# Performance work log

Hardware: AMD Instinct MI355X
Metric: run time of the kernel (lower is better)

The kernel has to match this reference:

```python
import jax, jax.numpy as jnp
import numpy as np

BLOCK_SIZE = 256


def setup_inputs() -> dict:
    key = jax.random.key(0)
    k1, k2, k3, k4 = jax.random.split(key, 4)
    B, T, C, H = 512, 256, 384, 64
    x = jax.random.normal(k1, (B, T, C), dtype=jnp.float32)
    Wk = jax.random.normal(k2, (H, C), dtype=jnp.float32) * (1.0 / np.sqrt(C))
    Wq = jax.random.normal(k3, (H, C), dtype=jnp.float32) * (1.0 / np.sqrt(C))
    Wv = jax.random.normal(k4, (H, C), dtype=jnp.float32) * (1.0 / np.sqrt(C))
    return {"x": x, "Wk": Wk, "Wq": Wq, "Wv": Wv}


def reference(x, Wk, Wq, Wv):
    # x: [B, T, C]; Wk/Wq/Wv: [H, C] (torch nn.Linear weight layout, bias=False)
    B, T, C = x.shape
    H = Wk.shape[0]
    k = jnp.einsum('btc,hc->bth', x, Wk)
    q = jnp.einsum('btc,hc->bth', x, Wq)
    v = jnp.einsum('btc,hc->bth', x, Wv)
    scale = 1.0 / jnp.sqrt(jnp.float32(H))
    scores = jnp.einsum('bqh,bkh->bqk', q, k) * scale  # [B, T, T]
    causal = jnp.tril(jnp.ones((T, T), dtype=bool))
    scores = jnp.where(causal, scores, -jnp.inf)
    weights = jax.nn.softmax(scores, axis=-1)
    # dropout is identity in eval mode
    out = jnp.einsum('bqk,bkh->bqh', weights, v)  # [B, T, H]
    return out
```

## Files before the change

kernel.cpp:

```cpp
#include <hip/hip_runtime.h>
#include <hip/hip_bf16.h>
#include <math.h>

#define TT 256
#define CC 384
#define HH 64

typedef float v4f   __attribute__((ext_vector_type(4)));
typedef short short8 __attribute__((ext_vector_type(8)));

#define MFMA(a, b, c) __builtin_amdgcn_mfma_f32_16x16x32_bf16((a), (b), (c), 0, 0, 0)

__device__ __forceinline__ unsigned short f2bf(float f) {
    unsigned int u = __float_as_uint(f);
    u += 0x7FFFu + ((u >> 16) & 1u);
    return (unsigned short)(u >> 16);
}

__device__ __forceinline__ ushort4 f2bf4(float4 f) {
    union { __hip_bfloat162 h2[2]; ushort4 u4; } cv;
    cv.h2[0] = __float22bfloat162_rn(make_float2(f.x, f.y));
    cv.h2[1] = __float22bfloat162_rn(make_float2(f.z, f.w));
    return cv.u4;
}

#define KLOOP_BARRIER() do {                                   \
    asm volatile("s_waitcnt lgkmcnt(0)" ::: "memory");         \
    __builtin_amdgcn_s_barrier();                              \
    __builtin_amdgcn_sched_barrier(0);                         \
} while (0)

#define QSCALE 0.18033688f

#define WST 0
#define KF  6144
#define VF  22528
#define SMU 38912

__global__ __launch_bounds__(512)
void prep_w(const float* __restrict__ Wkp, const float* __restrict__ Wqp,
            const float* __restrict__ Wvp, unsigned short* __restrict__ wf)
{
    const int idx  = blockIdx.x * 512 + threadIdx.x;
    const int lane = idx & 63;
    const int fn   = idx >> 6;
    const int nt   = fn % 12;
    const int s    = fn / 12;
    const int col  = lane & 15, quad = lane >> 4;
    const float* src = (nt < 4) ? Wqp : (nt < 8) ? Wkp : Wvp;
    const int h  = (nt & 3) * 16 + col;
    const int c0 = s * 32 + quad * 8;
    union { ushort4 u[2]; short8 s8; } pk;
    pk.u[0] = f2bf4(*(const float4*)(src + (size_t)h * CC + c0));
    pk.u[1] = f2bf4(*(const float4*)(src + (size_t)h * CC + c0 + 4));
    *(short8*)(wf + (size_t)idx * 8) = pk.s8;
}

__global__ __launch_bounds__(512, 4)
void fused_attn(const float* __restrict__ x, const unsigned short* __restrict__ wf,
                float* __restrict__ out)
{
    __shared__ unsigned short sm[SMU];
    const int tid  = threadIdx.x;
    const int wave = tid >> 6;
    const int lane = tid & 63;
    const int col  = lane & 15;
    const int quad = lane >> 4;
    const int b    = blockIdx.x;

    short8 aq0A, aq1A, aq0B, aq1B;

    #pragma unroll 1
    for (int half = 0; half < 2; ++half) {
        const int rb = half ? (7 - wave) : wave;
        const float* xrow = x + ((size_t)b * 256 + half * 128 + rb * 16 + col) * CC
                              + quad * 8;

        v4f acc[12];
        #pragma unroll
        for (int j = 0; j < 12; ++j) acc[j] = (v4f){0.f, 0.f, 0.f, 0.f};

        float4 xA0 = *(const float4*)(xrow);
        float4 xA1 = *(const float4*)(xrow + 4);
        short8 wA0 = *(const short8*)(wf + (size_t)tid * 8);
        short8 wA1;
        if (tid < 256) wA1 = *(const short8*)(wf + (size_t)(512 + tid) * 8);

        #pragma unroll
        for (int s = 0; s < 12; ++s) {
            float4 xB0, xB1; short8 wB0, wB1;
            if (s < 11) {
                xB0 = *(const float4*)(xrow + (s + 1) * 32);
                xB1 = *(const float4*)(xrow + (s + 1) * 32 + 4);
                wB0 = *(const short8*)(wf + ((size_t)(s + 1) * 768 + tid) * 8);
                if (tid < 256)
                    wB1 = *(const short8*)(wf + ((size_t)(s + 1) * 768 + 512 + tid) * 8);
            }
            KLOOP_BARRIER();
            *(short8*)&sm[WST + tid * 8] = wA0;
            if (tid < 256)
                *(short8*)&sm[WST + (512 + tid) * 8] = wA1;
            KLOOP_BARRIER();
            union { ushort4 u[2]; short8 s8; } pk;
            pk.u[0] = f2bf4(xA0); pk.u[1] = f2bf4(xA1);
            const short8 a = pk.s8;
            #pragma unroll
            for (int nt = 0; nt < 12; ++nt) {
                const short8 bf = *(const short8*)&sm[WST + (nt * 64 + lane) * 8];
                acc[nt] = MFMA(a, bf, acc[nt]);
            }
            if (s < 11) { xA0 = xB0; xA1 = xB1; wA0 = wB0; wA1 = wB1; }
        }

        const int kt = half ? (15 - wave) : wave;
        #pragma unroll
        for (int nt = 4; nt < 8; ++nt) {
            const int h = (nt - 4) * 16 + col;
            #pragma unroll
            for (int r = 0; r < 4; ++r)
                sm[KF + kt * 1024 + (h >> 3) * 128 + (quad * 4 + r) * 8 + (h & 7)]
                    = f2bf(acc[nt][r]);
        }
        #pragma unroll
        for (int nt = 8; nt < 12; ++nt) {
            const int h = (nt - 8) * 16 + col;
            #pragma unroll
            for (int r = 0; r < 4; ++r) {
                const int t = kt * 16 + quad * 4 + r;
                sm[VF + (h >> 4) * 4096 + (t >> 3) * 128 + (h & 15) * 8 + (t & 7)]
                    = f2bf(acc[nt][r]);
            }
        }
        __syncthreads();
        unsigned short* qs = sm + WST + wave * 512;
        #pragma unroll
        for (int nt = 0; nt < 2; ++nt)
            #pragma unroll
            for (int r = 0; r < 4; ++r)
                qs[(quad * 4 + r) * 32 + nt * 16 + col] = f2bf(acc[nt][r] * QSCALE);
        __threadfence_block();
        const short8 q0 = *(const short8*)&qs[col * 32 + quad * 8];
        __threadfence_block();
        #pragma unroll
        for (int nt = 2; nt < 4; ++nt)
            #pragma unroll
            for (int r = 0; r < 4; ++r)
                qs[(quad * 4 + r) * 32 + (nt - 2) * 16 + col] = f2bf(acc[nt][r] * QSCALE);
        __threadfence_block();
        const short8 q1 = *(const short8*)&qs[col * 32 + quad * 8];
        if (half == 0) { aq0A = q0; aq1A = q1; }
        else           { aq0B = q0; aq1B = q1; }
    }
    __syncthreads();

    unsigned short* Pb = sm + WST + wave * 640;

    #pragma unroll
    for (int mi = 0; mi < 2; ++mi) {
        const int qt = mi ? (15 - wave) : wave;
        const short8 aq0 = mi ? aq0B : aq0A;
        const short8 aq1 = mi ? aq1B : aq1A;

        float lsum[4];
        v4f oacc[4];
        #pragma unroll
        for (int r = 0; r < 4; ++r) lsum[r] = 0.f;
        #pragma unroll
        for (int hn = 0; hn < 4; ++hn) oacc[hn] = (v4f){0.f, 0.f, 0.f, 0.f};

        const int nch = qt / 2 + 1;
        short8 b00, b01, b10, b11;
        {
            const int t0 = KF + quad * 128 + col * 8;
            b00 = *(const short8*)&sm[t0];
            b01 = *(const short8*)&sm[t0 + 512];
            b10 = *(const short8*)&sm[t0 + 1024];
            b11 = *(const short8*)&sm[t0 + 1536];
        }
        for (int kc = 0; kc < nch; ++kc) {
            const int kb = kc * 32;
            v4f s0 = (v4f){0.f, 0.f, 0.f, 0.f};
            v4f s1 = (v4f){0.f, 0.f, 0.f, 0.f};
            s0 = MFMA(aq0, b00, s0);
            s0 = MFMA(aq1, b01, s0);
            s1 = MFMA(aq0, b10, s1);
            s1 = MFMA(aq1, b11, s1);
            if (kc + 1 < nch) {
                const int t0 = KF + (kc + 1) * 2048 + quad * 128 + col * 8;
                b00 = *(const short8*)&sm[t0];
                b01 = *(const short8*)&sm[t0 + 512];
                b10 = *(const short8*)&sm[t0 + 1024];
                b11 = *(const short8*)&sm[t0 + 1536];
            }
            const bool diag = (kc == qt / 2);
            #pragma unroll
            for (int r = 0; r < 4; ++r) {
                const int t = qt * 16 + quad * 4 + r;
                float v0 = s0[r];
                float v1 = s1[r];
                if (diag) {
                    if (kb + col > t)      v0 = -1e30f;
                    if (kb + 16 + col > t) v1 = -1e30f;
                }
                const float p0 = exp2f(v0);
                const float p1 = exp2f(v1);
                lsum[r] += p0 + p1;
                Pb[(quad * 4 + r) * 40 + col]      = f2bf(p0);
                Pb[(quad * 4 + r) * 40 + 16 + col] = f2bf(p1);
            }
            __threadfence_block();
            const short8 ap = *(const short8*)&Pb[col * 40 + quad * 8];
            #pragma unroll
            for (int hn = 0; hn < 4; ++hn) {
                const short8 bv = *(const short8*)&sm[VF + hn * 4096
                                        + (kc * 4 + quad) * 128 + col * 8];
                oacc[hn] = MFMA(ap, bv, oacc[hn]);
            }
        }

        #pragma unroll
        for (int r = 0; r < 4; ++r) {
            float l = lsum[r];
            l += __shfl_xor(l, 1);
            l += __shfl_xor(l, 2);
            l += __shfl_xor(l, 4);
            l += __shfl_xor(l, 8);
            const int t = qt * 16 + quad * 4 + r;
            const float inv = 1.0f / l;
            float* op = out + ((size_t)b * TT + t) * HH;
            #pragma unroll
            for (int hn = 0; hn < 4; ++hn)
                op[hn * 16 + col] = oacc[hn][r] * inv;
        }
    }
}

extern "C" void kernel_launch(void* const* d_in, const int* in_sizes, int n_in,
                              void* d_out, int out_size, void* d_ws, size_t ws_size,
                              hipStream_t stream) {
    const float* x  = (const float*)d_in[0];
    const float* Wk = (const float*)d_in[1];
    const float* Wq = (const float*)d_in[2];
    const float* Wv = (const float*)d_in[3];
    float* out = (float*)d_out;

    unsigned short* wf = (unsigned short*)d_ws;

    prep_w<<<dim3(18), dim3(512), 0, stream>>>(Wk, Wq, Wv, wf);
    fused_attn<<<dim3(512), dim3(512), 0, stream>>>(x, wf, out);
}
```

Measured before the change: 323.8 us.

## Compute QKV projection in one pass with two row tiles per wave

The projection GEMM now runs once instead of in two halves. Each wave handles two 16-row tiles, so every weight fragment read from shared memory feeds two MFMAs, and the per-step weight staging and barriers are paid once rather than twice. Q is written to a new shared-memory region and read back per query tile, replacing the in-register Q shuffle. This raises shared memory use and accumulator registers (launch bounds lowered to 2 blocks per SM), which reduces occupancy.

```diff
diff --git a/kernel.cpp b/kernel.cpp
--- a/kernel.cpp
+++ b/kernel.cpp
@@ -33,9 +33,10 @@
 #define QSCALE 0.18033688f
 
 #define WST 0
-#define KF  6144
-#define VF  22528
-#define SMU 38912
+#define QF  6144
+#define KF  22528
+#define VF  38912
+#define SMU 55296
 
 __global__ __launch_bounds__(512)
 void prep_w(const float* __restrict__ Wkp, const float* __restrict__ Wqp,
@@ -56,7 +57,7 @@
     *(short8*)(wf + (size_t)idx * 8) = pk.s8;
 }
 
-__global__ __launch_bounds__(512, 4)
+__global__ __launch_bounds__(512, 2)
 void fused_attn(const float* __restrict__ x, const unsigned short* __restrict__ wf,
                 float* __restrict__ out)
 {
@@ -68,88 +69,80 @@
     const int quad = lane >> 4;
     const int b    = blockIdx.x;
 
-    short8 aq0A, aq1A, aq0B, aq1B;
-
-    #pragma unroll 1
-    for (int half = 0; half < 2; ++half) {
-        const int rb = half ? (7 - wave) : wave;
-        const float* xrow = x + ((size_t)b * 256 + half * 128 + rb * 16 + col) * CC
-                              + quad * 8;
-
-        v4f acc[12];
-        #pragma unroll
-        for (int j = 0; j < 12; ++j) acc[j] = (v4f){0.f, 0.f, 0.f, 0.f};
-
-        float4 xA0 = *(const float4*)(xrow);
-        float4 xA1 = *(const float4*)(xrow + 4);
-        short8 wA0 = *(const short8*)(wf + (size_t)tid * 8);
-        short8 wA1;
-        if (tid < 256) wA1 = *(const short8*)(wf + (size_t)(512 + tid) * 8);
-
-        #pragma unroll
-        for (int s = 0; s < 12; ++s) {
-            float4 xB0, xB1; short8 wB0, wB1;
-            if (s < 11) {
-                xB0 = *(const float4*)(xrow + (s + 1) * 32);
-                xB1 = *(const float4*)(xrow + (s + 1) * 32 + 4);
-                wB0 = *(const short8*)(wf + ((size_t)(s + 1) * 768 + tid) * 8);
-                if (tid < 256)
-                    wB1 = *(const short8*)(wf + ((size_t)(s + 1) * 768 + 512 + tid) * 8);
-            }
-            KLOOP_BARRIER();
-            *(short8*)&sm[WST + tid * 8] = wA0;
+    const int rt0 = wave * 2;
+    const float* xr0 = x + ((size_t)b * 256 + rt0 * 16 + col) * CC + quad * 8;
+    const float* xr1 = xr0 + 16 * CC;
+
+    v4f acc[2][12];
+    #pragma unroll
+    for (int m = 0; m < 2; ++m)
+        #pragma unroll
+        for (int j = 0; j < 12; ++j) acc[m][j] = (v4f){0.f, 0.f, 0.f, 0.f};
+
+    float4 xA0 = *(const float4*)(xr0);
+    float4 xA1 = *(const float4*)(xr0 + 4);
+    float4 xA2 = *(const float4*)(xr1);
+    float4 xA3 = *(const float4*)(xr1 + 4);
+    short8 wA0 = *(const short8*)(wf + (size_t)tid * 8);
+    short8 wA1;
+    if (tid < 256) wA1 = *(const short8*)(wf + (size_t)(512 + tid) * 8);
+
+    #pragma unroll
+    for (int s = 0; s < 12; ++s) {
+        float4 xB0, xB1, xB2, xB3; short8 wB0, wB1;
+        if (s < 11) {
+            const int k0 = (s + 1) * 32;
+            xB0 = *(const float4*)(xr0 + k0);
+            xB1 = *(const float4*)(xr0 + k0 + 4);
+            xB2 = *(const float4*)(xr1 + k0);
+            xB3 = *(const float4*)(xr1 + k0 + 4);
+            wB0 = *(const short8*)(wf + ((size_t)(s + 1) * 768 + tid) * 8);
             if (tid < 256)
-                *(short8*)&sm[WST + (512 + tid) * 8] = wA1;
-            KLOOP_BARRIER();
-            union { ushort4 u[2]; short8 s8; } pk;
-            pk.u[0] = f2bf4(xA0); pk.u[1] = f2bf4(xA1);
-            const short8 a = pk.s8;
-            #pragma unroll
-            for (int nt = 0; nt < 12; ++nt) {
-                const short8 bf = *(const short8*)&sm[WST + (nt * 64 + lane) * 8];
-                acc[nt] = MFMA(a, bf, acc[nt]);
-            }
-            if (s < 11) { xA0 = xB0; xA1 = xB1; wA0 = wB0; wA1 = wB1; }
-        }
-
-        const int kt = half ? (15 - wave) : wave;
-        #pragma unroll
-        for (int nt = 4; nt < 8; ++nt) {
-            const int h = (nt - 4) * 16 + col;
-            #pragma unroll
-            for (int r = 0; r < 4; ++r)
-                sm[KF + kt * 1024 + (h >> 3) * 128 + (quad * 4 + r) * 8 + (h & 7)]
-                    = f2bf(acc[nt][r]);
-        }
-        #pragma unroll
-        for (int nt = 8; nt < 12; ++nt) {
-            const int h = (nt - 8) * 16 + col;
+                wB1 = *(const short8*)(wf + ((size_t)(s + 1) * 768 + 512 + tid) * 8);
+        }
+        KLOOP_BARRIER();
+        *(short8*)&sm[WST + tid * 8] = wA0;
+        if (tid < 256)
+            *(short8*)&sm[WST + (512 + tid) * 8] = wA1;
+        KLOOP_BARRIER();
+        union { ushort4 u[2]; short8 s8; } pk0, pk1;
+        pk0.u[0] = f2bf4(xA0); pk0.u[1] = f2bf4(xA1);
+        pk1.u[0] = f2bf4(xA2); pk1.u[1] = f2bf4(xA3);
+        const short8 a0 = pk0.s8, a1 = pk1.s8;
+        #pragma unroll
+        for (int nt = 0; nt < 12; ++nt) {
+            const short8 bf = *(const short8*)&sm[WST + (nt * 64 + lane) * 8];
+            acc[0][nt] = MFMA(a0, bf, acc[0][nt]);
+            acc[1][nt] = MFMA(a1, bf, acc[1][nt]);
+        }
+        if (s < 11) {
+            xA0 = xB0; xA1 = xB1; xA2 = xB2; xA3 = xB3;
+            wA0 = wB0; wA1 = wB1;
+        }
+    }
+
+    #pragma unroll
+    for (int m = 0; m < 2; ++m) {
+        const int qt = rt0 + m;
+        #pragma unroll
+        for (int nt = 0; nt < 12; ++nt) {
+            const int h = (nt & 3) * 16 + col;
             #pragma unroll
             for (int r = 0; r < 4; ++r) {
-                const int t = kt * 16 + quad * 4 + r;
-                sm[VF + (h >> 4) * 4096 + (t >> 3) * 128 + (h & 15) * 8 + (t & 7)]
-                    = f2bf(acc[nt][r]);
-            }
-        }
-        __syncthreads();
-        unsigned short* qs = sm + WST + wave * 512;
-        #pragma unroll
-        for (int nt = 0; nt < 2; ++nt)
-            #pragma unroll
-            for (int r = 0; r < 4; ++r)
-                qs[(quad * 4 + r) * 32 + nt * 16 + col] = f2bf(acc[nt][r] * QSCALE);
-        __threadfence_block();
-        const short8 q0 = *(const short8*)&qs[col * 32 + quad * 8];
-        __threadfence_block();
-        #pragma unroll
-        for (int nt = 2; nt < 4; ++nt)
-            #pragma unroll
-            for (int r = 0; r < 4; ++r)
-                qs[(quad * 4 + r) * 32 + (nt - 2) * 16 + col] = f2bf(acc[nt][r] * QSCALE);
-        __threadfence_block();
-        const short8 q1 = *(const short8*)&qs[col * 32 + quad * 8];
-        if (half == 0) { aq0A = q0; aq1A = q1; }
-        else           { aq0B = q0; aq1B = q1; }
+                const float v = acc[m][nt][r];
+                if (nt < 4) {
+                    sm[QF + qt * 1024 + (h >> 3) * 128 + (quad * 4 + r) * 8 + (h & 7)]
+                        = f2bf(v * QSCALE);
+                } else if (nt < 8) {
+                    sm[KF + qt * 1024 + (h >> 3) * 128 + (quad * 4 + r) * 8 + (h & 7)]
+                        = f2bf(v);
+                } else {
+                    const int t = qt * 16 + quad * 4 + r;
+                    sm[VF + (h >> 4) * 4096 + (t >> 3) * 128 + (h & 15) * 8 + (t & 7)]
+                        = f2bf(v);
+                }
+            }
+        }
     }
     __syncthreads();
 
@@ -158,8 +151,8 @@
     #pragma unroll
     for (int mi = 0; mi < 2; ++mi) {
         const int qt = mi ? (15 - wave) : wave;
-        const short8 aq0 = mi ? aq0B : aq0A;
-        const short8 aq1 = mi ? aq1B : aq1A;
+        const short8 aq0 = *(const short8*)&sm[QF + qt * 1024 + quad * 128 + col * 8];
+        const short8 aq1 = *(const short8*)&sm[QF + qt * 1024 + 512 + quad * 128 + col * 8];
 
         float lsum[4];
         v4f oacc[4];
```

Measured after the change: 304.8 us. 5.9% less time.

## Use 16 waves per block, one query tile each, weights read from global

Applied to the files above, without the earlier changes.

Grows the block to 1024 threads so each of 16 waves owns a single 16-row tile, removing the two-half loop. The projection GEMM now reads bf16 weight fragments straight from global memory (cache) instead of staging them through LDS behind two barriers per k-step. Causal work is no longer balanced by pairing tiles, so late waves carry more attention chunks, and occupancy depends on register pressure at 1024 threads.

```diff
diff --git a/kernel.cpp b/kernel.cpp
--- a/kernel.cpp
+++ b/kernel.cpp
@@ -24,18 +24,12 @@
     return cv.u4;
 }
 
-#define KLOOP_BARRIER() do {                                   \
-    asm volatile("s_waitcnt lgkmcnt(0)" ::: "memory");         \
-    __builtin_amdgcn_s_barrier();                              \
-    __builtin_amdgcn_sched_barrier(0);                         \
-} while (0)
-
 #define QSCALE 0.18033688f
 
-#define WST 0
-#define KF  6144
-#define VF  22528
-#define SMU 38912
+#define PB  0
+#define KF  10240
+#define VF  26624
+#define SMU 43008
 
 __global__ __launch_bounds__(512)
 void prep_w(const float* __restrict__ Wkp, const float* __restrict__ Wqp,
@@ -56,7 +50,7 @@
     *(short8*)(wf + (size_t)idx * 8) = pk.s8;
 }
 
-__global__ __launch_bounds__(512, 4)
+__global__ __launch_bounds__(1024, 4)
 void fused_attn(const float* __restrict__ x, const unsigned short* __restrict__ wf,
                 float* __restrict__ out)
 {
@@ -68,170 +62,145 @@
     const int quad = lane >> 4;
     const int b    = blockIdx.x;
 
-    short8 aq0A, aq1A, aq0B, aq1B;
+    const float* xr = x + ((size_t)b * 256 + wave * 16 + col) * CC + quad * 8;
+
+    v4f acc[12];
+    #pragma unroll
+    for (int j = 0; j < 12; ++j) acc[j] = (v4f){0.f, 0.f, 0.f, 0.f};
+
+    float4 xA0 = *(const float4*)(xr);
+    float4 xA1 = *(const float4*)(xr + 4);
 
     #pragma unroll 1
-    for (int half = 0; half < 2; ++half) {
-        const int rb = half ? (7 - wave) : wave;
-        const float* xrow = x + ((size_t)b * 256 + half * 128 + rb * 16 + col) * CC
-                              + quad * 8;
-
-        v4f acc[12];
-        #pragma unroll
-        for (int j = 0; j < 12; ++j) acc[j] = (v4f){0.f, 0.f, 0.f, 0.f};
-
-        float4 xA0 = *(const float4*)(xrow);
-        float4 xA1 = *(const float4*)(xrow + 4);
-        short8 wA0 = *(const short8*)(wf + (size_t)tid * 8);
-        short8 wA1;
-        if (tid < 256) wA1 = *(const short8*)(wf + (size_t)(512 + tid) * 8);
-
-        #pragma unroll
-        for (int s = 0; s < 12; ++s) {
-            float4 xB0, xB1; short8 wB0, wB1;
-            if (s < 11) {
-                xB0 = *(const float4*)(xrow + (s + 1) * 32);
-                xB1 = *(const float4*)(xrow + (s + 1) * 32 + 4);
-                wB0 = *(const short8*)(wf + ((size_t)(s + 1) * 768 + tid) * 8);
-                if (tid < 256)
-                    wB1 = *(const short8*)(wf + ((size_t)(s + 1) * 768 + 512 + tid) * 8);
-            }
-            KLOOP_BARRIER();
-            *(short8*)&sm[WST + tid * 8] = wA0;
-            if (tid < 256)
-                *(short8*)&sm[WST + (512 + tid) * 8] = wA1;
-            KLOOP_BARRIER();
-            union { ushort4 u[2]; short8 s8; } pk;
-            pk.u[0] = f2bf4(xA0); pk.u[1] = f2bf4(xA1);
-            const short8 a = pk.s8;
-            #pragma unroll
-            for (int nt = 0; nt < 12; ++nt) {
-                const short8 bf = *(const short8*)&sm[WST + (nt * 64 + lane) * 8];
-                acc[nt] = MFMA(a, bf, acc[nt]);
-            }
-            if (s < 11) { xA0 = xB0; xA1 = xB1; wA0 = wB0; wA1 = wB1; }
-        }
-
-        const int kt = half ? (15 - wave) : wave;
-        #pragma unroll
-        for (int nt = 4; nt < 8; ++nt) {
-            const int h = (nt - 4) * 16 + col;
-            #pragma unroll
-            for (int r = 0; r < 4; ++r)
-                sm[KF + kt * 1024 + (h >> 3) * 128 + (quad * 4 + r) * 8 + (h & 7)]
-                    = f2bf(acc[nt][r]);
-        }
-        #pragma unroll
-        for (int nt = 8; nt < 12; ++nt) {
-            const int h = (nt - 8) * 16 + col;
-            #pragma unroll
-            for (int r = 0; r < 4; ++r) {
-                const int t = kt * 16 + quad * 4 + r;
-                sm[VF + (h >> 4) * 4096 + (t >> 3) * 128 + (h & 15) * 8 + (t & 7)]
-                    = f2bf(acc[nt][r]);
-            }
-        }
-        __syncthreads();
-        unsigned short* qs = sm + WST + wave * 512;
-        #pragma unroll
-        for (int nt = 0; nt < 2; ++nt)
-            #pragma unroll
-            for (int r = 0; r < 4; ++r)
-                qs[(quad * 4 + r) * 32 + nt * 16 + col] = f2bf(acc[nt][r] * QSCALE);
-        __threadfence_block();
-        const short8 q0 = *(const short8*)&qs[col * 32 + quad * 8];
-        __threadfence_block();
-        #pragma unroll
-        for (int nt = 2; nt < 4; ++nt)
-            #pragma unroll
-            for (int r = 0; r < 4; ++r)
-                qs[(quad * 4 + r) * 32 + (nt - 2) * 16 + col] = f2bf(acc[nt][r] * QSCALE);
-        __threadfence_block();
-        const short8 q1 = *(const short8*)&qs[col * 32 + quad * 8];
-        if (half == 0) { aq0A = q0; aq1A = q1; }
-        else           { aq0B = q0; aq1B = q1; }
-    }
+    for (int s = 0; s < 12; ++s) {
+        float4 xB0, xB1;
+        if (s < 11) {
+            const int k0 = (s + 1) * 32;
+            xB0 = *(const float4*)(xr + k0);
+            xB1 = *(const float4*)(xr + k0 + 4);
+        }
+        union { ushort4 u[2]; short8 s8; } pk;
+        pk.u[0] = f2bf4(xA0); pk.u[1] = f2bf4(xA1);
+        const short8 a = pk.s8;
+        const unsigned short* wstep = wf + (size_t)s * 768 * 8 + lane * 8;
+        #pragma unroll
+        for (int nt = 0; nt < 12; ++nt) {
+            const short8 bf = *(const short8*)(wstep + nt * 512);
+            acc[nt] = MFMA(a, bf, acc[nt]);
+        }
+        if (s < 11) { xA0 = xB0; xA1 = xB1; }
+    }
+
+    const int qt = wave;
+    #pragma unroll
+    for (int nt = 4; nt < 8; ++nt) {
+        const int h = (nt - 4) * 16 + col;
+        #pragma unroll
+        for (int r = 0; r < 4; ++r)
+            sm[KF + qt * 1024 + (h >> 3) * 128 + (quad * 4 + r) * 8 + (h & 7)]
+                = f2bf(acc[nt][r]);
+    }
+    #pragma unroll
+    for (int nt = 8; nt < 12; ++nt) {
+        const int h = (nt - 8) * 16 + col;
+        #pragma unroll
+        for (int r = 0; r < 4; ++r) {
+            const int t = qt * 16 + quad * 4 + r;
+            sm[VF + (h >> 4) * 4096 + (t >> 3) * 128 + (h & 15) * 8 + (t & 7)]
+                = f2bf(acc[nt][r]);
+        }
+    }
+    unsigned short* qs = sm + PB + wave * 640;
+    #pragma unroll
+    for (int nt = 0; nt < 2; ++nt)
+        #pragma unroll
+        for (int r = 0; r < 4; ++r)
+            qs[(quad * 4 + r) * 32 + nt * 16 + col] = f2bf(acc[nt][r] * QSCALE);
+    __threadfence_block();
+    const short8 aq0 = *(const short8*)&qs[col * 32 + quad * 8];
+    __threadfence_block();
+    #pragma unroll
+    for (int nt = 2; nt < 4; ++nt)
+        #pragma unroll
+        for (int r = 0; r < 4; ++r)
+            qs[(quad * 4 + r) * 32 + (nt - 2) * 16 + col] = f2bf(acc[nt][r] * QSCALE);
+    __threadfence_block();
+    const short8 aq1 = *(const short8*)&qs[col * 32 + quad * 8];
+
     __syncthreads();
 
-    unsigned short* Pb = sm + WST + wave * 640;
-
-    #pragma unroll
-    for (int mi = 0; mi < 2; ++mi) {
-        const int qt = mi ? (15 - wave) : wave;
-        const short8 aq0 = mi ? aq0B : aq0A;
-        const short8 aq1 = mi ? aq1B : aq1A;
-
-        float lsum[4];
-        v4f oacc[4];
-        #pragma unroll
-        for (int r = 0; r < 4; ++r) lsum[r] = 0.f;
-        #pragma unroll
-        for (int hn = 0; hn < 4; ++hn) oacc[hn] = (v4f){0.f, 0.f, 0.f, 0.f};
-
-        const int nch = qt / 2 + 1;
-        short8 b00, b01, b10, b11;
-        {
-            const int t0 = KF + quad * 128 + col * 8;
+    unsigned short* Pb = sm + PB + wave * 640;
+
+    float lsum[4];
+    v4f oacc[4];
+    #pragma unroll
+    for (int r = 0; r < 4; ++r) lsum[r] = 0.f;
+    #pragma unroll
+    for (int hn = 0; hn < 4; ++hn) oacc[hn] = (v4f){0.f, 0.f, 0.f, 0.f};
+
+    const int nch = qt / 2 + 1;
+    short8 b00, b01, b10, b11;
+    {
+        const int t0 = KF + quad * 128 + col * 8;
+        b00 = *(const short8*)&sm[t0];
+        b01 = *(const short8*)&sm[t0 + 512];
+        b10 = *(const short8*)&sm[t0 + 1024];
+        b11 = *(const short8*)&sm[t0 + 1536];
+    }
+    for (int kc = 0; kc < nch; ++kc) {
+        const int kb = kc * 32;
+        v4f s0 = (v4f){0.f, 0.f, 0.f, 0.f};
+        v4f s1 = (v4f){0.f, 0.f, 0.f, 0.f};
+        s0 = MFMA(aq0, b00, s0);
+        s0 = MFMA(aq1, b01, s0);
+        s1 = MFMA(aq0, b10, s1);
+        s1 = MFMA(aq1, b11, s1);
+        if (kc + 1 < nch) {
+            const int t0 = KF + (kc + 1) * 2048 + quad * 128 + col * 8;
             b00 = *(const short8*)&sm[t0];
             b01 = *(const short8*)&sm[t0 + 512];
             b10 = *(const short8*)&sm[t0 + 1024];
             b11 = *(const short8*)&sm[t0 + 1536];
         }
-        for (int kc = 0; kc < nch; ++kc) {
-            const int kb = kc * 32;
-            v4f s0 = (v4f){0.f, 0.f, 0.f, 0.f};
-            v4f s1 = (v4f){0.f, 0.f, 0.f, 0.f};
-            s0 = MFMA(aq0, b00, s0);
-            s0 = MFMA(aq1, b01, s0);
-            s1 = MFMA(aq0, b10, s1);
-            s1 = MFMA(aq1, b11, s1);
-            if (kc + 1 < nch) {
-                const int t0 = KF + (kc + 1) * 2048 + quad * 128 + col * 8;
-                b00 = *(const short8*)&sm[t0];
-                b01 = *(const short8*)&sm[t0 + 512];
-                b10 = *(const short8*)&sm[t0 + 1024];
-                b11 = *(const short8*)&sm[t0 + 1536];
+        const bool diag = (kc == qt / 2);
+        #pragma unroll
+        for (int r = 0; r < 4; ++r) {
+            const int t = qt * 16 + quad * 4 + r;
+            float v0 = s0[r];
+            float v1 = s1[r];
+            if (diag) {
+                if (kb + col > t)      v0 = -1e30f;
+                if (kb + 16 + col > t) v1 = -1e30f;
             }
-            const bool diag = (kc == qt / 2);
-            #pragma unroll
-            for (int r = 0; r < 4; ++r) {
-                const int t = qt * 16 + quad * 4 + r;
-                float v0 = s0[r];
-                float v1 = s1[r];
-                if (diag) {
-                    if (kb + col > t)      v0 = -1e30f;
-                    if (kb + 16 + col > t) v1 = -1e30f;
-                }
-                const float p0 = exp2f(v0);
-                const float p1 = exp2f(v1);
-                lsum[r] += p0 + p1;
-                Pb[(quad * 4 + r) * 40 + col]      = f2bf(p0);
-                Pb[(quad * 4 + r) * 40 + 16 + col] = f2bf(p1);
-            }
-            __threadfence_block();
-            const short8 ap = *(const short8*)&Pb[col * 40 + quad * 8];
-            #pragma unroll
-            for (int hn = 0; hn < 4; ++hn) {
-                const short8 bv = *(const short8*)&sm[VF + hn * 4096
-                                        + (kc * 4 + quad) * 128 + col * 8];
-                oacc[hn] = MFMA(ap, bv, oacc[hn]);
-            }
-        }
-
-        #pragma unroll
-        for (int r = 0; r < 4; ++r) {
-            float l = lsum[r];
-            l += __shfl_xor(l, 1);
-            l += __shfl_xor(l, 2);
-            l += __shfl_xor(l, 4);
-            l += __shfl_xor(l, 8);
-            const int t = qt * 16 + quad * 4 + r;
-            const float inv = 1.0f / l;
-            float* op = out + ((size_t)b * TT + t) * HH;
-            #pragma unroll
-            for (int hn = 0; hn < 4; ++hn)
-                op[hn * 16 + col] = oacc[hn][r] * inv;
-        }
+            const float p0 = exp2f(v0);
+            const float p1 = exp2f(v1);
+            lsum[r] += p0 + p1;
+            Pb[(quad * 4 + r) * 40 + col]      = f2bf(p0);
+            Pb[(quad * 4 + r) * 40 + 16 + col] = f2bf(p1);
+        }
+        __threadfence_block();
+        const short8 ap = *(const short8*)&Pb[col * 40 + quad * 8];
+        #pragma unroll
+        for (int hn = 0; hn < 4; ++hn) {
+            const short8 bv = *(const short8*)&sm[VF + hn * 4096
+                                    + (kc * 4 + quad) * 128 + col * 8];
+            oacc[hn] = MFMA(ap, bv, oacc[hn]);
+        }
+    }
+
+    #pragma unroll
+    for (int r = 0; r < 4; ++r) {
+        float l = lsum[r];
+        l += __shfl_xor(l, 1);
+        l += __shfl_xor(l, 2);
+        l += __shfl_xor(l, 4);
+        l += __shfl_xor(l, 8);
+        const int t = qt * 16 + quad * 4 + r;
+        const float inv = 1.0f / l;
+        float* op = out + ((size_t)b * TT + t) * HH;
+        #pragma unroll
+        for (int hn = 0; hn < 4; ++hn)
+            op[hn * 16 + col] = oacc[hn][r] * inv;
     }
 }
 
@@ -247,5 +216,5 @@
     unsigned short* wf = (unsigned short*)d_ws;
 
     prep_w<<<dim3(18), dim3(512), 0, stream>>>(Wk, Wq, Wv, wf);
-    fused_attn<<<dim3(512), dim3(512), 0, stream>>>(x, wf, out);
-}
+    fused_attn<<<dim3(512), dim3(1024), 0, stream>>>(x, wf, out);
+}
```

Measured after the change: 326.5 us. About the same (+0.8%).
